# Performance work log

Hardware: AMD Instinct MI355X
Metric: run time of the kernel (lower is better)

The kernel has to match this reference:

```python
import jax, jax.numpy as jnp
import numpy as np

U = 256   # units
D = 256   # input_dim
B = 65536 # batch


def hard_tanh(x):
    return jnp.clip(x, -1.0, 1.0)


def binarize(x):
    # sign quantization (forward); straight-through in the bwd module
    return jnp.where(x >= 0, 1.0, -1.0).astype(x.dtype)


def setup_inputs() -> dict:
    key = jax.random.key(0)
    k1, k2, k3, k4, k5 = jax.random.split(key, 5)
    return {
        "inputs": jax.random.normal(k1, (B, D), dtype=jnp.float32),
        "h": jax.random.normal(k2, (B, U), dtype=jnp.float32),
        "c": jax.random.normal(k3, (B, U), dtype=jnp.float32),
        "kernel": jax.random.normal(k4, (D, 4 * U), dtype=jnp.float32) * 0.05,
        "recurrent_kernel": jax.random.normal(k5, (U, 4 * U), dtype=jnp.float32) * 0.05,
    }


def reference(inputs, h, c, kernel, recurrent_kernel):
    u = kernel.shape[1] // 4
    h_tm1 = hard_tanh(h)
    c_tm1 = hard_tanh(c)
    # binarized input projection, hard_tanh applied to each gate pre-activation
    x_all = hard_tanh(inputs @ binarize(kernel))            # [B, 4U]
    x_i, x_f, x_c, x_o = (x_all[:, :u], x_all[:, u:2*u],
                          x_all[:, 2*u:3*u], x_all[:, 3*u:])
    # binarized recurrent projection
    r_all = h_tm1 @ binarize(recurrent_kernel)              # [B, 4U]
    r_i, r_f, r_c, r_o = (r_all[:, :u], r_all[:, u:2*u],
                          r_all[:, 2*u:3*u], r_all[:, 3*u:])
    # NOTE: faithful to source: f pairs x_i with W_f, i pairs x_f with W_i
    f = hard_tanh(x_i + r_f)
    i = hard_tanh(x_f + r_i)
    c_new = f * c_tm1 + i * hard_tanh(x_c + r_c)
    o = hard_tanh(x_o + r_o)
    h_new = hard_tanh(o * hard_tanh(c_new))
    return (h_new, h_new, c_new)
```

## Files before the change

kernel.cpp:

```cpp
#include <hip/hip_runtime.h>


#define NB 65536

typedef _Float16 f16x8 __attribute__((ext_vector_type(8)));
typedef float f32x16 __attribute__((ext_vector_type(16)));

__device__ __forceinline__ float htanh(float x) { return fminf(1.f, fmaxf(-1.f, x)); }

__global__ void prep_w(const float* __restrict__ Kf, const float* __restrict__ RKf,
                       unsigned short* __restrict__ wfrag) {
  __shared__ unsigned short sgn[32][72];
  const int b = blockIdx.x;
  const int side = b >> 7, kt = (b >> 4) & 7, nt = b & 15;
  const float* M = side ? RKf : Kf;
  const int t = threadIdx.x;

  {
    const int k = t >> 3, n8 = (t & 7) << 3;
    const float* p = M + (kt * 32 + k) * 1024 + nt * 64 + n8;
    float4 v0 = *(const float4*)p;
    float4 v1 = *(const float4*)(p + 4);
    float xs[8] = {v0.x, v0.y, v0.z, v0.w, v1.x, v1.y, v1.z, v1.w};
#pragma unroll
    for (int i = 0; i < 8; ++i)
      sgn[k][n8 + i] = (xs[i] >= 0.f) ? 0x3C00u : 0xBC00u;
  }
  __syncthreads();

  const int fl = t >> 6, l = t & 63;
  const int j = fl >> 1, uh = fl & 1;
  const int nloc = uh * 32 + (l & 31);
  const int kloc = j * 16 + (l >> 5) * 8;
  unsigned short o[8];
#pragma unroll
  for (int e = 0; e < 8; ++e) o[e] = sgn[kloc + e][nloc];
  const int ng = nt * 64 + nloc;
  const int gate = ng >> 8, u32 = (ng >> 5) & 7;
  const int fragid = (((kt * 2 + j) * 2 + side) * 4 + gate) * 8 + u32;
  uint4 ov;
  ov.x = (unsigned)o[0] | ((unsigned)o[1] << 16);
  ov.y = (unsigned)o[2] | ((unsigned)o[3] << 16);
  ov.z = (unsigned)o[4] | ((unsigned)o[5] << 16);
  ov.w = (unsigned)o[6] | ((unsigned)o[7] << 16);
  *(uint4*)((char*)wfrag + fragid * 1024 + l * 16) = ov;
}

__global__ __launch_bounds__(256, 3)
void blstm_main(const float* __restrict__ xin, const float* __restrict__ hin,
                const float* __restrict__ cin, const unsigned short* __restrict__ wfrag,
                float* __restrict__ out) {
  __shared__ char smem[32768];

  const int bid = blockIdx.x;
  const int swz = (bid & 7) * 1024 + (bid >> 3);
  const int mb = swz >> 2, ub = swz & 3;
  const int m0 = mb << 5;
  const int u0 = ub << 6;

  const int tid = threadIdx.x;
  const int lane = tid & 63;
  const int w = tid >> 6;
  const int wu = w & 1, wg = w >> 1;
  const int l31 = lane & 31, lh = lane >> 5;

  const int sSide = tid >> 7;
  const int sRow = (tid & 127) >> 2;
  const int sQ = tid & 3;
  const float* aPtr = (sSide ? hin : xin) + (m0 + sRow) * 256 + (sQ << 3);
  char* const aWr = smem + sSide * 4096 + sRow * 128;
  const int swzHi = ((sQ ^ (sRow & 7)) << 4);
  const int swzLo = (((sQ + 4) ^ (sRow & 7)) << 4);

  const char* const wbase = (const char*)wfrag + lane * 16;

  f32x16 acc[4] = {};

  float4 a0 = *(const float4*)(aPtr);
  float4 a1 = *(const float4*)(aPtr + 4);

  for (int s = 0; s < 8; ++s) {
    {
      char* wr = aWr + (s & 1) * 8192;
      float xs[8] = {a0.x, a0.y, a0.z, a0.w, a1.x, a1.y, a1.z, a1.w};
      f16x8 hv, lv;
#pragma unroll
      for (int i = 0; i < 8; ++i) {
        float x = xs[i];
        if (sSide) x = htanh(x);
        _Float16 hf = (_Float16)x;
        hv[i] = hf;
        lv[i] = (_Float16)(x - (float)hf);
      }
      *(f16x8*)(wr + swzHi) = hv;
      *(f16x8*)(wr + swzLo) = lv;
    }

    f16x8 wfr[2][4];
#pragma unroll
    for (int j = 0; j < 2; ++j)
#pragma unroll
      for (int nf = 0; nf < 4; ++nf) {
        const int side = nf >> 1, gate = wg * 2 + (nf & 1);
        const int fragid = (((s * 2 + j) * 2 + side) * 4 + gate) * 8 + (ub * 2 + wu);
        wfr[j][nf] = *(const f16x8*)(wbase + fragid * 1024);
      }
    if (s < 7) {
      a0 = *(const float4*)(aPtr + (s + 1) * 32);
      a1 = *(const float4*)(aPtr + (s + 1) * 32 + 4);
    }

    __syncthreads();

    const char* rd = smem + (s & 1) * 8192;
#pragma unroll
    for (int j = 0; j < 2; ++j) {
#pragma unroll
      for (int hl = 0; hl < 2; ++hl) {
        f16x8 af[2];
#pragma unroll
        for (int side = 0; side < 2; ++side)
          af[side] = *(const f16x8*)(rd + side * 4096 + l31 * 128 +
                       ((((hl << 2) | (j << 1) | lh) ^ (l31 & 7)) << 4));
#pragma unroll
        for (int nf = 0; nf < 4; ++nf)
          acc[nf] = __builtin_amdgcn_mfma_f32_32x32x16_f16(af[nf >> 1], wfr[j][nf],
                                                           acc[nf], 0, 0, 0);
      }
    }
  }

  float* ex = (float*)(smem + 16384 + wu * 8192);

  if (wg == 1) {
    float4 c4[4], o4[4];
#pragma unroll
    for (int r = 0; r < 16; ++r) {
      float cand = htanh(htanh(acc[0][r]) + acc[2][r]);
      float og   = htanh(htanh(acc[1][r]) + acc[3][r]);
      ((float*)&c4[r >> 2])[r & 3] = cand;
      ((float*)&o4[r >> 2])[r & 3] = og;
    }
#pragma unroll
    for (int c = 0; c < 4; ++c) {
      *(float4*)((char*)ex + c * 1024 + lane * 16) = c4[c];
      *(float4*)((char*)ex + 4096 + c * 1024 + lane * 16) = o4[c];
    }
  }
  __syncthreads();
  if (wg == 0) {
    float4 c4[4], o4[4];
#pragma unroll
    for (int c = 0; c < 4; ++c) {
      c4[c] = *(const float4*)((const char*)ex + c * 1024 + lane * 16);
      o4[c] = *(const float4*)((const char*)ex + 4096 + c * 1024 + lane * 16);
    }
#pragma unroll
    for (int r = 0; r < 16; ++r) {
      const int row = (r & 3) + ((r >> 2) << 3) + (lh << 2);
      const int grow = m0 + row;
      const int gu = u0 + wu * 32 + l31;
      const float fg = htanh(htanh(acc[0][r]) + acc[3][r]);
      const float ig = htanh(htanh(acc[1][r]) + acc[2][r]);
      const float cand = ((const float*)&c4[r >> 2])[r & 3];
      const float og   = ((const float*)&o4[r >> 2])[r & 3];
      const float ct = htanh(cin[grow * 256 + gu]);
      const float cn = fg * ct + ig * cand;
      const float hn = htanh(og * htanh(cn));
      const int o1 = grow * 256 + gu;
      out[o1] = hn;
      out[NB * 256 + o1] = hn;
      out[2 * NB * 256 + o1] = cn;
    }
  }
}

extern "C" void kernel_launch(void* const* d_in, const int* in_sizes, int n_in,
                              void* d_out, int out_size, void* d_ws, size_t ws_size,
                              hipStream_t stream) {
  const float* xin = (const float*)d_in[0];
  const float* hin = (const float*)d_in[1];
  const float* cin = (const float*)d_in[2];
  const float* kf  = (const float*)d_in[3];
  const float* rkf = (const float*)d_in[4];
  float* out = (float*)d_out;

  unsigned short* wfrag = (unsigned short*)d_ws;

  prep_w<<<256, 256, 0, stream>>>(kf, rkf, wfrag);
  blstm_main<<<8192, 256, 0, stream>>>(xin, hin, cin, wfrag, out);
}
```

Measured before the change: 204.3 us.

## Split activation conversion into prep kernel and persistent register-resident GEMM

Adds a prep_a kernel that converts inputs and hard_tanh(h) into hi/lo fp16 MFMA fragment images in workspace. The main kernel becomes a persistent-style GEMM with 1024 blocks of 512 threads. Each wave keeps its weight fragments in registers across 8 row chunks and streams A fragments straight from global memory with double buffering, exchanging gate results through LDS. The weight fragment order is changed to suit this, and hard_tanh now uses fmed3. The cost is an extra round trip of the activation image (fp16 hi+lo, the same byte count as the fp32 source) through global memory, in exchange for removing LDS staging and the per-block reconversion.

```diff
diff --git a/kernel.cpp b/kernel.cpp
--- a/kernel.cpp
+++ b/kernel.cpp
@@ -4,9 +4,12 @@
 #define NB 65536
 
 typedef _Float16 f16x8 __attribute__((ext_vector_type(8)));
+typedef __fp16 fp16x2 __attribute__((ext_vector_type(2)));
 typedef float f32x16 __attribute__((ext_vector_type(16)));
 
-__device__ __forceinline__ float htanh(float x) { return fminf(1.f, fmaxf(-1.f, x)); }
+__device__ __forceinline__ float htanh(float x) {
+  return __builtin_amdgcn_fmed3f(x, -1.0f, 1.0f);
+}
 
 __global__ void prep_w(const float* __restrict__ Kf, const float* __restrict__ RKf,
                        unsigned short* __restrict__ wfrag) {
@@ -15,7 +18,6 @@
   const int side = b >> 7, kt = (b >> 4) & 7, nt = b & 15;
   const float* M = side ? RKf : Kf;
   const int t = threadIdx.x;
-
   {
     const int k = t >> 3, n8 = (t & 7) << 3;
     const float* p = M + (kt * 32 + k) * 1024 + nt * 64 + n8;
@@ -27,17 +29,17 @@
       sgn[k][n8 + i] = (xs[i] >= 0.f) ? 0x3C00u : 0xBC00u;
   }
   __syncthreads();
-
   const int fl = t >> 6, l = t & 63;
-  const int j = fl >> 1, uh = fl & 1;
-  const int nloc = uh * 32 + (l & 31);
+  const int j = fl >> 1, uhh = fl & 1;
+  const int nloc = uhh * 32 + (l & 31);
   const int kloc = j * 16 + (l >> 5) * 8;
   unsigned short o[8];
 #pragma unroll
   for (int e = 0; e < 8; ++e) o[e] = sgn[kloc + e][nloc];
   const int ng = nt * 64 + nloc;
   const int gate = ng >> 8, u32 = (ng >> 5) & 7;
-  const int fragid = (((kt * 2 + j) * 2 + side) * 4 + gate) * 8 + u32;
+  const int k16 = kt * 2 + j;
+  const int fragid = ((k16 * 2 + side) * 8 + u32) * 4 + gate;
   uint4 ov;
   ov.x = (unsigned)o[0] | ((unsigned)o[1] << 16);
   ov.y = (unsigned)o[2] | ((unsigned)o[3] << 16);
@@ -46,133 +48,190 @@
   *(uint4*)((char*)wfrag + fragid * 1024 + l * 16) = ov;
 }
 
-__global__ __launch_bounds__(256, 3)
-void blstm_main(const float* __restrict__ xin, const float* __restrict__ hin,
-                const float* __restrict__ cin, const unsigned short* __restrict__ wfrag,
-                float* __restrict__ out) {
-  __shared__ char smem[32768];
+__global__ __launch_bounds__(256)
+void prep_a(const float* __restrict__ xin, const float* __restrict__ hin,
+            char* __restrict__ aimg) {
+  __shared__ float tile[32][68];
+  const int b = blockIdx.x;
+  const int side = b & 1, kq = (b >> 1) & 3, strip = b >> 3;
+  const float* src = side ? hin : xin;
+  const int t = threadIdx.x;
+  {
+    const int row = t >> 3, kc = (t & 7) << 3;
+    const float* p = src + (strip * 32 + row) * 256 + kq * 64 + kc;
+    float4 v0 = *(const float4*)p;
+    float4 v1 = *(const float4*)(p + 4);
+    *(float4*)&tile[row][kc] = v0;
+    *(float4*)&tile[row][kc + 4] = v1;
+  }
+  __syncthreads();
+  const int w = t >> 6, l = t & 63;
+  const int l31 = l & 31, lh = l >> 5;
+  const int k16 = kq * 4 + w;
+  const int c0 = w * 16 + lh * 8;
+  float4 u0 = *(const float4*)&tile[l31][c0];
+  float4 u1 = *(const float4*)&tile[l31][c0 + 4];
+  float v0 = u0.x, v1 = u0.y, v2 = u0.z, v3 = u0.w;
+  float v4 = u1.x, v5 = u1.y, v6 = u1.z, v7 = u1.w;
+  if (side) {
+    v0 = htanh(v0); v1 = htanh(v1); v2 = htanh(v2); v3 = htanh(v3);
+    v4 = htanh(v4); v5 = htanh(v5); v6 = htanh(v6); v7 = htanh(v7);
+  }
+  fp16x2 h01 = __builtin_amdgcn_cvt_pkrtz(v0, v1);
+  fp16x2 h23 = __builtin_amdgcn_cvt_pkrtz(v2, v3);
+  fp16x2 h45 = __builtin_amdgcn_cvt_pkrtz(v4, v5);
+  fp16x2 h67 = __builtin_amdgcn_cvt_pkrtz(v6, v7);
+  fp16x2 l01 = __builtin_amdgcn_cvt_pkrtz(v0 - (float)h01[0], v1 - (float)h01[1]);
+  fp16x2 l23 = __builtin_amdgcn_cvt_pkrtz(v2 - (float)h23[0], v3 - (float)h23[1]);
+  fp16x2 l45 = __builtin_amdgcn_cvt_pkrtz(v4 - (float)h45[0], v5 - (float)h45[1]);
+  fp16x2 l67 = __builtin_amdgcn_cvt_pkrtz(v6 - (float)h67[0], v7 - (float)h67[1]);
+  uint4 H, L;
+  H.x = __builtin_bit_cast(unsigned, h01); H.y = __builtin_bit_cast(unsigned, h23);
+  H.z = __builtin_bit_cast(unsigned, h45); H.w = __builtin_bit_cast(unsigned, h67);
+  L.x = __builtin_bit_cast(unsigned, l01); L.y = __builtin_bit_cast(unsigned, l23);
+  L.z = __builtin_bit_cast(unsigned, l45); L.w = __builtin_bit_cast(unsigned, l67);
+  char* dst = aimg + (size_t)(((strip * 16 + k16) * 2 + side) * 2) * 1024 + l * 16;
+  *(uint4*)dst = H;
+  *(uint4*)(dst + 1024) = L;
+}
+
+__global__ __launch_bounds__(512, 4)
+void blstm_gemm(const char* __restrict__ aimg, const unsigned short* __restrict__ wfrag,
+                const float* __restrict__ cin, float* __restrict__ out) {
+  __shared__ char ex[65536];
 
   const int bid = blockIdx.x;
-  const int swz = (bid & 7) * 1024 + (bid >> 3);
-  const int mb = swz >> 2, ub = swz & 3;
-  const int m0 = mb << 5;
-  const int u0 = ub << 6;
-
-  const int tid = threadIdx.x;
-  const int lane = tid & 63;
-  const int w = tid >> 6;
-  const int wu = w & 1, wg = w >> 1;
+  const int xcd = bid & 7, j = bid >> 3;
+  const int U = j & 7, g8 = j >> 3;
+  const int tid = threadIdx.x, lane = tid & 63, w = tid >> 6;
+  const int s = w & 1, gate = w >> 1;
   const int l31 = lane & 31, lh = lane >> 5;
 
-  const int sSide = tid >> 7;
-  const int sRow = (tid & 127) >> 2;
-  const int sQ = tid & 3;
-  const float* aPtr = (sSide ? hin : xin) + (m0 + sRow) * 256 + (sQ << 3);
-  char* const aWr = smem + sSide * 4096 + sRow * 128;
-  const int swzHi = ((sQ ^ (sRow & 7)) << 4);
-  const int swzLo = (((sQ + 4) ^ (sRow & 7)) << 4);
-
-  const char* const wbase = (const char*)wfrag + lane * 16;
-
-  f32x16 acc[4] = {};
-
-  float4 a0 = *(const float4*)(aPtr);
-  float4 a1 = *(const float4*)(aPtr + 4);
-
-  for (int s = 0; s < 8; ++s) {
-    {
-      char* wr = aWr + (s & 1) * 8192;
-      float xs[8] = {a0.x, a0.y, a0.z, a0.w, a1.x, a1.y, a1.z, a1.w};
-      f16x8 hv, lv;
-#pragma unroll
-      for (int i = 0; i < 8; ++i) {
-        float x = xs[i];
-        if (sSide) x = htanh(x);
-        _Float16 hf = (_Float16)x;
-        hv[i] = hf;
-        lv[i] = (_Float16)(x - (float)hf);
+  const char* wb = (const char*)wfrag + s * 32768 + U * 4096 + gate * 1024 + lane * 16;
+  const char* ab0 = aimg + s * 2048 + lane * 16;
+
+  const int chunk0 = xcd * 128 + g8 * 8;
+
+  f16x8 wreg[8];
+  f32x16 acc[2];
+  f16x8 a0h, a0l, a1h, a1l, b0h, b0l, b1h, b1l;
+
+#define AADDR(C, ST, K, T) (ab0 + (size_t)((C) * 2 + (ST)) * 65536 + (K) * 4096 + (T) * 1024)
+
+#pragma unroll
+  for (int k = 0; k < 8; ++k) wreg[k] = *(const f16x8*)(wb + k * 65536);
+  a0h = *(const f16x8*)AADDR(chunk0, 0, 0, 0);
+  a0l = *(const f16x8*)AADDR(chunk0, 0, 0, 1);
+  a1h = *(const f16x8*)AADDR(chunk0, 1, 0, 0);
+  a1l = *(const f16x8*)AADDR(chunk0, 1, 0, 1);
+
+#define MFMA_STEP(CH0, CL0, CH1, CL1, WF) do {                                \
+    acc[0] = __builtin_amdgcn_mfma_f32_32x32x16_f16(CH0, WF, acc[0], 0, 0, 0); \
+    acc[0] = __builtin_amdgcn_mfma_f32_32x32x16_f16(CL0, WF, acc[0], 0, 0, 0); \
+    acc[1] = __builtin_amdgcn_mfma_f32_32x32x16_f16(CH1, WF, acc[1], 0, 0, 0); \
+    acc[1] = __builtin_amdgcn_mfma_f32_32x32x16_f16(CL1, WF, acc[1], 0, 0, 0); \
+  } while (0)
+
+#define KS(K, C0H, C0L, C1H, C1L, N0H, N0L, N1H, N1L) do {                    \
+    if ((K) < 15) {                                                           \
+      N0H = *(const f16x8*)AADDR(chunk, 0, (K) + 1, 0);                       \
+      N0L = *(const f16x8*)AADDR(chunk, 0, (K) + 1, 1);                       \
+      N1H = *(const f16x8*)AADDR(chunk, 1, (K) + 1, 0);                       \
+      N1L = *(const f16x8*)AADDR(chunk, 1, (K) + 1, 1);                       \
+    } else if (t < 7) {                                                       \
+      N0H = *(const f16x8*)AADDR(chunk + 1, 0, 0, 0);                         \
+      N0L = *(const f16x8*)AADDR(chunk + 1, 0, 0, 1);                         \
+      N1H = *(const f16x8*)AADDR(chunk + 1, 1, 0, 0);                         \
+      N1L = *(const f16x8*)AADDR(chunk + 1, 1, 0, 1);                         \
+    }                                                                         \
+    MFMA_STEP(C0H, C0L, C1H, C1L, wreg[(K) & 7]);                             \
+    if ((K) == 7) {                                                           \
+      _Pragma("unroll")                                                       \
+      for (int kk = 0; kk < 8; ++kk)                                          \
+        wreg[kk] = *(const f16x8*)(wb + (8 + kk) * 65536);                    \
+    }                                                                         \
+    if ((K) == 15 && t < 7) {                                                 \
+      _Pragma("unroll")                                                       \
+      for (int kk = 0; kk < 8; ++kk)                                          \
+        wreg[kk] = *(const f16x8*)(wb + kk * 65536);                          \
+    }                                                                         \
+  } while (0)
+
+#pragma unroll 1
+  for (int t = 0; t < 8; ++t) {
+    const int chunk = chunk0 + t;
+    const int m0 = chunk * 64;
+    const f32x16 zacc = {};
+    acc[0] = zacc;
+    acc[1] = zacc;
+
+    KS(0,  a0h, a0l, a1h, a1l,  b0h, b0l, b1h, b1l);
+    KS(1,  b0h, b0l, b1h, b1l,  a0h, a0l, a1h, a1l);
+    KS(2,  a0h, a0l, a1h, a1l,  b0h, b0l, b1h, b1l);
+    KS(3,  b0h, b0l, b1h, b1l,  a0h, a0l, a1h, a1l);
+    KS(4,  a0h, a0l, a1h, a1l,  b0h, b0l, b1h, b1l);
+    KS(5,  b0h, b0l, b1h, b1l,  a0h, a0l, a1h, a1l);
+    KS(6,  a0h, a0l, a1h, a1l,  b0h, b0l, b1h, b1l);
+    KS(7,  b0h, b0l, b1h, b1l,  a0h, a0l, a1h, a1l);
+    KS(8,  a0h, a0l, a1h, a1l,  b0h, b0l, b1h, b1l);
+    KS(9,  b0h, b0l, b1h, b1l,  a0h, a0l, a1h, a1l);
+    KS(10, a0h, a0l, a1h, a1l,  b0h, b0l, b1h, b1l);
+    KS(11, b0h, b0l, b1h, b1l,  a0h, a0l, a1h, a1l);
+    KS(12, a0h, a0l, a1h, a1l,  b0h, b0l, b1h, b1l);
+    KS(13, b0h, b0l, b1h, b1l,  a0h, a0l, a1h, a1l);
+    KS(14, a0h, a0l, a1h, a1l,  b0h, b0l, b1h, b1l);
+    KS(15, b0h, b0l, b1h, b1l,  a0h, a0l, a1h, a1l);
+
+    const int Rb = w * 8 + lh * 4;
+    float ct0 = cin[(m0 + Rb + 0) * 256 + U * 32 + l31];
+    float ct1 = cin[(m0 + Rb + 1) * 256 + U * 32 + l31];
+    float ct2 = cin[(m0 + Rb + 2) * 256 + U * 32 + l31];
+    float ct3 = cin[(m0 + Rb + 3) * 256 + U * 32 + l31];
+
+    asm volatile("s_waitcnt lgkmcnt(0)\n\ts_barrier" ::: "memory");
+#pragma unroll
+    for (int st = 0; st < 2; ++st)
+#pragma unroll
+      for (int q = 0; q < 4; ++q) {
+        float4 v;
+        v.x = acc[st][q * 4 + 0]; v.y = acc[st][q * 4 + 1];
+        v.z = acc[st][q * 4 + 2]; v.w = acc[st][q * 4 + 3];
+        *(float4*)(ex + w * 8192 + st * 4096 + q * 1024 + lane * 16) = v;
       }
-      *(f16x8*)(wr + swzHi) = hv;
-      *(f16x8*)(wr + swzLo) = lv;
+    asm volatile("s_waitcnt lgkmcnt(0)\n\ts_barrier" ::: "memory");
+
+    float cts[4] = {ct0, ct1, ct2, ct3};
+#pragma unroll
+    for (int i = 0; i < 4; ++i) {
+      const int R = Rb + i;
+      const int st = R >> 5, r32 = R & 31;
+      const int q = r32 >> 3, el = r32 & 3;
+      const int sl = l31 + ((r32 >> 2) & 1) * 32;
+      const int off = st * 4096 + q * 1024 + sl * 16 + el * 4;
+      const float xi = htanh(*(const float*)(ex + 0 * 8192 + off));
+      const float ri =        *(const float*)(ex + 1 * 8192 + off);
+      const float xf = htanh(*(const float*)(ex + 2 * 8192 + off));
+      const float rf =        *(const float*)(ex + 3 * 8192 + off);
+      const float xc = htanh(*(const float*)(ex + 4 * 8192 + off));
+      const float rc =        *(const float*)(ex + 5 * 8192 + off);
+      const float xo = htanh(*(const float*)(ex + 6 * 8192 + off));
+      const float ro =        *(const float*)(ex + 7 * 8192 + off);
+      const float fg   = htanh(xi + rf);
+      const float ig   = htanh(xf + ri);
+      const float cand = htanh(xc + rc);
+      const float og   = htanh(xo + ro);
+      const float c0 = htanh(cts[i]);
+      const float cn = fg * c0 + ig * cand;
+      const float hn = htanh(og * htanh(cn));
+      const int o1 = (m0 + R) * 256 + U * 32 + l31;
+      out[o1] = hn;
+      out[16777216 + o1] = hn;
+      out[33554432 + o1] = cn;
     }
-
-    f16x8 wfr[2][4];
-#pragma unroll
-    for (int j = 0; j < 2; ++j)
-#pragma unroll
-      for (int nf = 0; nf < 4; ++nf) {
-        const int side = nf >> 1, gate = wg * 2 + (nf & 1);
-        const int fragid = (((s * 2 + j) * 2 + side) * 4 + gate) * 8 + (ub * 2 + wu);
-        wfr[j][nf] = *(const f16x8*)(wbase + fragid * 1024);
-      }
-    if (s < 7) {
-      a0 = *(const float4*)(aPtr + (s + 1) * 32);
-      a1 = *(const float4*)(aPtr + (s + 1) * 32 + 4);
-    }
-
-    __syncthreads();
-
-    const char* rd = smem + (s & 1) * 8192;
-#pragma unroll
-    for (int j = 0; j < 2; ++j) {
-#pragma unroll
-      for (int hl = 0; hl < 2; ++hl) {
-        f16x8 af[2];
-#pragma unroll
-        for (int side = 0; side < 2; ++side)
-          af[side] = *(const f16x8*)(rd + side * 4096 + l31 * 128 +
-                       ((((hl << 2) | (j << 1) | lh) ^ (l31 & 7)) << 4));
-#pragma unroll
-        for (int nf = 0; nf < 4; ++nf)
-          acc[nf] = __builtin_amdgcn_mfma_f32_32x32x16_f16(af[nf >> 1], wfr[j][nf],
-                                                           acc[nf], 0, 0, 0);
-      }
-    }
-  }
-
-  float* ex = (float*)(smem + 16384 + wu * 8192);
-
-  if (wg == 1) {
-    float4 c4[4], o4[4];
-#pragma unroll
-    for (int r = 0; r < 16; ++r) {
-      float cand = htanh(htanh(acc[0][r]) + acc[2][r]);
-      float og   = htanh(htanh(acc[1][r]) + acc[3][r]);
-      ((float*)&c4[r >> 2])[r & 3] = cand;
-      ((float*)&o4[r >> 2])[r & 3] = og;
-    }
-#pragma unroll
-    for (int c = 0; c < 4; ++c) {
-      *(float4*)((char*)ex + c * 1024 + lane * 16) = c4[c];
-      *(float4*)((char*)ex + 4096 + c * 1024 + lane * 16) = o4[c];
-    }
-  }
-  __syncthreads();
-  if (wg == 0) {
-    float4 c4[4], o4[4];
-#pragma unroll
-    for (int c = 0; c < 4; ++c) {
-      c4[c] = *(const float4*)((const char*)ex + c * 1024 + lane * 16);
-      o4[c] = *(const float4*)((const char*)ex + 4096 + c * 1024 + lane * 16);
-    }
-#pragma unroll
-    for (int r = 0; r < 16; ++r) {
-      const int row = (r & 3) + ((r >> 2) << 3) + (lh << 2);
-      const int grow = m0 + row;
-      const int gu = u0 + wu * 32 + l31;
-      const float fg = htanh(htanh(acc[0][r]) + acc[3][r]);
-      const float ig = htanh(htanh(acc[1][r]) + acc[2][r]);
-      const float cand = ((const float*)&c4[r >> 2])[r & 3];
-      const float og   = ((const float*)&o4[r >> 2])[r & 3];
-      const float ct = htanh(cin[grow * 256 + gu]);
-      const float cn = fg * ct + ig * cand;
-      const float hn = htanh(og * htanh(cn));
-      const int o1 = grow * 256 + gu;
-      out[o1] = hn;
-      out[NB * 256 + o1] = hn;
-      out[2 * NB * 256 + o1] = cn;
-    }
-  }
+  }
+#undef KS
+#undef MFMA_STEP
+#undef AADDR
 }
 
 extern "C" void kernel_launch(void* const* d_in, const int* in_sizes, int n_in,
@@ -186,7 +245,9 @@
   float* out = (float*)d_out;
 
   unsigned short* wfrag = (unsigned short*)d_ws;
+  char* aimg = (char*)d_ws + (1 << 20);
 
   prep_w<<<256, 256, 0, stream>>>(kf, rkf, wfrag);
-  blstm_main<<<8192, 256, 0, stream>>>(xin, hin, cin, wfrag, out);
-}
+  prep_a<<<16384, 256, 0, stream>>>(xin, hin, aimg);
+  blstm_gemm<<<1024, 512, 0, stream>>>(aimg, wfrag, cin, out);
+}
```

Measured after the change: 541.5 us. 165% more time.

## Rewrite fused BLSTM GEMM with 64-row tiles, persistent loop, register double-buffered weights

Applied to the files above, without the earlier changes.

Replaces the main kernel with a version that processes 64-row M tiles (two per block over a persistent loop of 2048 blocks), double-buffers the weight fragments in registers and the activation tiles in shared memory, and uses packed fp16 conversion, fmed3 clamping, setprio around MFMA bursts and raw barriers. The gate-exchange epilogue is reorganized so the other wave group computes the output and prefetches c earlier. The goal is better weight reuse per load, fewer launched blocks, and overlap of global loads with MFMA work. In exchange it uses more LDS and registers, which lowers occupancy to 2 blocks per SM, and it uses round-toward-zero packing for the hi/lo fp16 split.

```diff
diff --git a/kernel.cpp b/kernel.cpp
--- a/kernel.cpp
+++ b/kernel.cpp
@@ -4,9 +4,17 @@
 #define NB 65536
 
 typedef _Float16 f16x8 __attribute__((ext_vector_type(8)));
+typedef __fp16 fp16x2 __attribute__((ext_vector_type(2)));
 typedef float f32x16 __attribute__((ext_vector_type(16)));
 
-__device__ __forceinline__ float htanh(float x) { return fminf(1.f, fmaxf(-1.f, x)); }
+__device__ __forceinline__ float htanh(float x) {
+  return __builtin_amdgcn_fmed3f(x, -1.0f, 1.0f);
+}
+
+__device__ __forceinline__ unsigned pk2(float a, float b) {
+  fp16x2 p = __builtin_amdgcn_cvt_pkrtz(a, b);
+  return __builtin_bit_cast(unsigned, p);
+}
 
 __global__ void prep_w(const float* __restrict__ Kf, const float* __restrict__ RKf,
                        unsigned short* __restrict__ wfrag) {
@@ -15,7 +23,6 @@
   const int side = b >> 7, kt = (b >> 4) & 7, nt = b & 15;
   const float* M = side ? RKf : Kf;
   const int t = threadIdx.x;
-
   {
     const int k = t >> 3, n8 = (t & 7) << 3;
     const float* p = M + (kt * 32 + k) * 1024 + nt * 64 + n8;
@@ -27,17 +34,17 @@
       sgn[k][n8 + i] = (xs[i] >= 0.f) ? 0x3C00u : 0xBC00u;
   }
   __syncthreads();
-
   const int fl = t >> 6, l = t & 63;
-  const int j = fl >> 1, uh = fl & 1;
-  const int nloc = uh * 32 + (l & 31);
+  const int j = fl >> 1, uhh = fl & 1;
+  const int nloc = uhh * 32 + (l & 31);
   const int kloc = j * 16 + (l >> 5) * 8;
   unsigned short o[8];
 #pragma unroll
   for (int e = 0; e < 8; ++e) o[e] = sgn[kloc + e][nloc];
   const int ng = nt * 64 + nloc;
   const int gate = ng >> 8, u32 = (ng >> 5) & 7;
-  const int fragid = (((kt * 2 + j) * 2 + side) * 4 + gate) * 8 + u32;
+  const int k16 = kt * 2 + j;
+  const int fragid = ((k16 * 2 + side) * 8 + u32) * 4 + gate;
   uint4 ov;
   ov.x = (unsigned)o[0] | ((unsigned)o[1] << 16);
   ov.y = (unsigned)o[2] | ((unsigned)o[3] << 16);
@@ -46,133 +53,196 @@
   *(uint4*)((char*)wfrag + fragid * 1024 + l * 16) = ov;
 }
 
-__global__ __launch_bounds__(256, 3)
-void blstm_main(const float* __restrict__ xin, const float* __restrict__ hin,
+__global__ __launch_bounds__(256, 2)
+void blstm_gemm(const float* __restrict__ xin, const float* __restrict__ hin,
                 const float* __restrict__ cin, const unsigned short* __restrict__ wfrag,
                 float* __restrict__ out) {
-  __shared__ char smem[32768];
+  __shared__ char smem[65536];
 
   const int bid = blockIdx.x;
-  const int swz = (bid & 7) * 1024 + (bid >> 3);
-  const int mb = swz >> 2, ub = swz & 3;
-  const int m0 = mb << 5;
-  const int u0 = ub << 6;
-
-  const int tid = threadIdx.x;
-  const int lane = tid & 63;
-  const int w = tid >> 6;
-  const int wu = w & 1, wg = w >> 1;
+  const int swz = (bid & 7) * 256 + (bid >> 3);
+  const int U = swz & 3;
+  const int mg = swz >> 2;
+
+  const int tid = threadIdx.x, lane = tid & 63, w = tid >> 6;
+  const int gp = w >> 1, uhf = w & 1;
   const int l31 = lane & 31, lh = lane >> 5;
 
   const int sSide = tid >> 7;
-  const int sRow = (tid & 127) >> 2;
-  const int sQ = tid & 3;
-  const float* aPtr = (sSide ? hin : xin) + (m0 + sRow) * 256 + (sQ << 3);
-  char* const aWr = smem + sSide * 4096 + sRow * 128;
-  const int swzHi = ((sQ ^ (sRow & 7)) << 4);
-  const int swzLo = (((sQ + 4) ^ (sRow & 7)) << 4);
-
-  const char* const wbase = (const char*)wfrag + lane * 16;
-
-  f32x16 acc[4] = {};
-
-  float4 a0 = *(const float4*)(aPtr);
-  float4 a1 = *(const float4*)(aPtr + 4);
-
-  for (int s = 0; s < 8; ++s) {
-    {
-      char* wr = aWr + (s & 1) * 8192;
-      float xs[8] = {a0.x, a0.y, a0.z, a0.w, a1.x, a1.y, a1.z, a1.w};
-      f16x8 hv, lv;
-#pragma unroll
-      for (int i = 0; i < 8; ++i) {
-        float x = xs[i];
-        if (sSide) x = htanh(x);
-        _Float16 hf = (_Float16)x;
-        hv[i] = hf;
-        lv[i] = (_Float16)(x - (float)hf);
-      }
-      *(f16x8*)(wr + swzHi) = hv;
-      *(f16x8*)(wr + swzLo) = lv;
+  const int sRow = (tid & 127) >> 1;
+  const int sKh = tid & 1;
+  const float* const aP0 = (sSide ? hin : xin) + (size_t)sRow * 256 + sKh * 16;
+  char* const swr = smem +
+      ((((sKh * 2 + sSide) * 2 + (sRow >> 5)) * 2) * 1024) + (sRow & 31) * 16;
+
+  const char* const wq = (const char*)wfrag + lane * 16;
+  int wbOff[4];
+#pragma unroll
+  for (int nf = 0; nf < 4; ++nf) {
+    const int side = nf >> 1, gate = gp * 2 + (nf & 1);
+    wbOff[nf] = (side * 32 + (U * 2 + uhf) * 4 + gate) * 1024;
+  }
+
+  f32x16 acc[2][4];
+  f16x8 wA[8], wB[8];
+  float4 av0, av1, av2, av3;
+
+#pragma unroll
+  for (int j = 0; j < 2; ++j)
+#pragma unroll
+    for (int nf = 0; nf < 4; ++nf)
+      wA[j * 4 + nf] = *(const f16x8*)(wq + (0 + j) * 65536 + wbOff[nf]);
+
+#define CVT_STORE(B) do {                                                    \
+    float e_[16] = {av0.x, av0.y, av0.z, av0.w, av1.x, av1.y, av1.z, av1.w,  \
+                    av2.x, av2.y, av2.z, av2.w, av3.x, av3.y, av3.z, av3.w}; \
+    if (sSide) {                                                             \
+      _Pragma("unroll") for (int i_ = 0; i_ < 16; ++i_) e_[i_] = htanh(e_[i_]); \
+    }                                                                        \
+    unsigned hw_[8], lw_[8];                                                 \
+    _Pragma("unroll")                                                        \
+    for (int i_ = 0; i_ < 8; ++i_) {                                         \
+      fp16x2 h_ = __builtin_amdgcn_cvt_pkrtz(e_[2 * i_], e_[2 * i_ + 1]);    \
+      hw_[i_] = __builtin_bit_cast(unsigned, h_);                            \
+      lw_[i_] = pk2(e_[2 * i_] - (float)h_[0], e_[2 * i_ + 1] - (float)h_[1]); \
+    }                                                                        \
+    char* wp_ = swr + (B) * 16384;                                           \
+    *(uint4*)(wp_)        = make_uint4(hw_[0], hw_[1], hw_[2], hw_[3]);      \
+    *(uint4*)(wp_ + 512)  = make_uint4(hw_[4], hw_[5], hw_[6], hw_[7]);      \
+    *(uint4*)(wp_ + 1024) = make_uint4(lw_[0], lw_[1], lw_[2], lw_[3]);      \
+    *(uint4*)(wp_ + 1536) = make_uint4(lw_[4], lw_[5], lw_[6], lw_[7]);      \
+  } while (0)
+
+#define K16(J, WARR, RB) do {                                                \
+    _Pragma("unroll")                                                        \
+    for (int sd_ = 0; sd_ < 2; ++sd_) {                                      \
+      _Pragma("unroll")                                                      \
+      for (int st_ = 0; st_ < 2; ++st_) {                                    \
+        f16x8 ah_ = *(const f16x8*)((RB) + (J) * 8192 + sd_ * 4096 + st_ * 2048); \
+        f16x8 al_ = *(const f16x8*)((RB) + (J) * 8192 + sd_ * 4096 + st_ * 2048 + 1024); \
+        acc[st_][sd_ * 2 + 0] = __builtin_amdgcn_mfma_f32_32x32x16_f16(      \
+            ah_, WARR[(J) * 4 + sd_ * 2 + 0], acc[st_][sd_ * 2 + 0], 0, 0, 0); \
+        acc[st_][sd_ * 2 + 1] = __builtin_amdgcn_mfma_f32_32x32x16_f16(      \
+            ah_, WARR[(J) * 4 + sd_ * 2 + 1], acc[st_][sd_ * 2 + 1], 0, 0, 0); \
+        acc[st_][sd_ * 2 + 0] = __builtin_amdgcn_mfma_f32_32x32x16_f16(      \
+            al_, WARR[(J) * 4 + sd_ * 2 + 0], acc[st_][sd_ * 2 + 0], 0, 0, 0); \
+        acc[st_][sd_ * 2 + 1] = __builtin_amdgcn_mfma_f32_32x32x16_f16(      \
+            al_, WARR[(J) * 4 + sd_ * 2 + 1], acc[st_][sd_ * 2 + 1], 0, 0, 0); \
+      }                                                                      \
+    }                                                                        \
+  } while (0)
+
+#define STEP(S, WCUR, WNXT, LAST) do {                                       \
+    asm volatile("s_waitcnt lgkmcnt(0)\n\ts_barrier" ::: "memory");          \
+    if (!(LAST)) {                                                           \
+      av0 = *(const float4*)(aPc + ((S) + 1) * 32);                          \
+      av1 = *(const float4*)(aPc + ((S) + 1) * 32 + 4);                      \
+      av2 = *(const float4*)(aPc + ((S) + 1) * 32 + 8);                      \
+      av3 = *(const float4*)(aPc + ((S) + 1) * 32 + 12);                     \
+    }                                                                        \
+    _Pragma("unroll")                                                        \
+    for (int j_ = 0; j_ < 2; ++j_)                                           \
+      _Pragma("unroll")                                                      \
+      for (int nf_ = 0; nf_ < 4; ++nf_)                                      \
+        WNXT[j_ * 4 + nf_] = *(const f16x8*)(                                \
+            wq + (((((S) + 1) & 7) * 2) + j_) * 65536 + wbOff[nf_]);         \
+    {                                                                        \
+      const char* rb_ = smem + ((S) & 1) * 16384 + lane * 16;                \
+      __builtin_amdgcn_s_setprio(1);                                         \
+      K16(0, WCUR, rb_);                                                     \
+      K16(1, WCUR, rb_);                                                     \
+      __builtin_amdgcn_s_setprio(0);                                         \
+    }                                                                        \
+    if (!(LAST)) CVT_STORE(((S) + 1) & 1);                                   \
+  } while (0)
+
+  float* ex = (float*)(smem + 32768);
+
+#pragma unroll 1
+  for (int c = 0; c < 2; ++c) {
+    const int m0 = (mg + c * 512) * 64;
+    const float* aPc = aP0 + (size_t)m0 * 256;
+
+    const f32x16 z = {};
+#pragma unroll
+    for (int st = 0; st < 2; ++st)
+#pragma unroll
+      for (int nf = 0; nf < 4; ++nf) acc[st][nf] = z;
+
+    av0 = *(const float4*)(aPc);
+    av1 = *(const float4*)(aPc + 4);
+    av2 = *(const float4*)(aPc + 8);
+    av3 = *(const float4*)(aPc + 12);
+    CVT_STORE(0);
+
+    STEP(0, wA, wB, false);
+    STEP(1, wB, wA, false);
+    STEP(2, wA, wB, false);
+    STEP(3, wB, wA, false);
+    STEP(4, wA, wB, false);
+    STEP(5, wB, wA, false);
+    STEP(6, wA, wB, false);
+    STEP(7, wB, wA, true);
+
+    const int uc = U * 64 + uhf * 32 + l31;
+    float cins[32];
+    if (gp == 1) {
+#pragma unroll
+      for (int st = 0; st < 2; ++st)
+#pragma unroll
+        for (int q = 0; q < 4; ++q)
+#pragma unroll
+          for (int i = 0; i < 4; ++i) {
+            const int row = st * 32 + 8 * q + 4 * lh + i;
+            cins[(st * 4 + q) * 4 + i] = cin[(size_t)(m0 + row) * 256 + uc];
+          }
     }
-
-    f16x8 wfr[2][4];
-#pragma unroll
-    for (int j = 0; j < 2; ++j)
-#pragma unroll
-      for (int nf = 0; nf < 4; ++nf) {
-        const int side = nf >> 1, gate = wg * 2 + (nf & 1);
-        const int fragid = (((s * 2 + j) * 2 + side) * 4 + gate) * 8 + (ub * 2 + wu);
-        wfr[j][nf] = *(const f16x8*)(wbase + fragid * 1024);
-      }
-    if (s < 7) {
-      a0 = *(const float4*)(aPtr + (s + 1) * 32);
-      a1 = *(const float4*)(aPtr + (s + 1) * 32 + 4);
+    if (gp == 0) {
+#pragma unroll
+      for (int st = 0; st < 2; ++st)
+#pragma unroll
+        for (int q = 0; q < 4; ++q) {
+          float4 fv, iv;
+#pragma unroll
+          for (int i = 0; i < 4; ++i) {
+            const int r = q * 4 + i;
+            ((float*)&fv)[i] = htanh(htanh(acc[st][0][r]) + acc[st][3][r]);
+            ((float*)&iv)[i] = htanh(htanh(acc[st][1][r]) + acc[st][2][r]);
+          }
+          *(float4*)((char*)ex + (((uhf * 2 + 0) * 2 + st) * 4096) + q * 1024 + lane * 16) = fv;
+          *(float4*)((char*)ex + (((uhf * 2 + 1) * 2 + st) * 4096) + q * 1024 + lane * 16) = iv;
+        }
     }
-
-    __syncthreads();
-
-    const char* rd = smem + (s & 1) * 8192;
-#pragma unroll
-    for (int j = 0; j < 2; ++j) {
-#pragma unroll
-      for (int hl = 0; hl < 2; ++hl) {
-        f16x8 af[2];
-#pragma unroll
-        for (int side = 0; side < 2; ++side)
-          af[side] = *(const f16x8*)(rd + side * 4096 + l31 * 128 +
-                       ((((hl << 2) | (j << 1) | lh) ^ (l31 & 7)) << 4));
-#pragma unroll
-        for (int nf = 0; nf < 4; ++nf)
-          acc[nf] = __builtin_amdgcn_mfma_f32_32x32x16_f16(af[nf >> 1], wfr[j][nf],
-                                                           acc[nf], 0, 0, 0);
-      }
+    asm volatile("s_waitcnt lgkmcnt(0)\n\ts_barrier" ::: "memory");
+    if (gp == 1) {
+#pragma unroll
+      for (int st = 0; st < 2; ++st)
+#pragma unroll
+        for (int q = 0; q < 4; ++q) {
+          float4 fv = *(const float4*)((char*)ex + (((uhf * 2 + 0) * 2 + st) * 4096) + q * 1024 + lane * 16);
+          float4 iv = *(const float4*)((char*)ex + (((uhf * 2 + 1) * 2 + st) * 4096) + q * 1024 + lane * 16);
+#pragma unroll
+          for (int i = 0; i < 4; ++i) {
+            const int r = q * 4 + i;
+            const float cand = htanh(htanh(acc[st][0][r]) + acc[st][2][r]);
+            const float og   = htanh(htanh(acc[st][1][r]) + acc[st][3][r]);
+            const float fg = ((const float*)&fv)[i];
+            const float ig = ((const float*)&iv)[i];
+            const float ct = htanh(cins[(st * 4 + q) * 4 + i]);
+            const float cn = fg * ct + ig * cand;
+            const float hn = htanh(og * htanh(cn));
+            const int row = st * 32 + 8 * q + 4 * lh + i;
+            const size_t o1 = (size_t)(m0 + row) * 256 + uc;
+            out[o1] = hn;
+            out[(size_t)NB * 256 + o1] = hn;
+            out[2 * (size_t)NB * 256 + o1] = cn;
+          }
+        }
     }
   }
-
-  float* ex = (float*)(smem + 16384 + wu * 8192);
-
-  if (wg == 1) {
-    float4 c4[4], o4[4];
-#pragma unroll
-    for (int r = 0; r < 16; ++r) {
-      float cand = htanh(htanh(acc[0][r]) + acc[2][r]);
-      float og   = htanh(htanh(acc[1][r]) + acc[3][r]);
-      ((float*)&c4[r >> 2])[r & 3] = cand;
-      ((float*)&o4[r >> 2])[r & 3] = og;
-    }
-#pragma unroll
-    for (int c = 0; c < 4; ++c) {
-      *(float4*)((char*)ex + c * 1024 + lane * 16) = c4[c];
-      *(float4*)((char*)ex + 4096 + c * 1024 + lane * 16) = o4[c];
-    }
-  }
-  __syncthreads();
-  if (wg == 0) {
-    float4 c4[4], o4[4];
-#pragma unroll
-    for (int c = 0; c < 4; ++c) {
-      c4[c] = *(const float4*)((const char*)ex + c * 1024 + lane * 16);
-      o4[c] = *(const float4*)((const char*)ex + 4096 + c * 1024 + lane * 16);
-    }
-#pragma unroll
-    for (int r = 0; r < 16; ++r) {
-      const int row = (r & 3) + ((r >> 2) << 3) + (lh << 2);
-      const int grow = m0 + row;
-      const int gu = u0 + wu * 32 + l31;
-      const float fg = htanh(htanh(acc[0][r]) + acc[3][r]);
-      const float ig = htanh(htanh(acc[1][r]) + acc[2][r]);
-      const float cand = ((const float*)&c4[r >> 2])[r & 3];
-      const float og   = ((const float*)&o4[r >> 2])[r & 3];
-      const float ct = htanh(cin[grow * 256 + gu]);
-      const float cn = fg * ct + ig * cand;
-      const float hn = htanh(og * htanh(cn));
-      const int o1 = grow * 256 + gu;
-      out[o1] = hn;
-      out[NB * 256 + o1] = hn;
-      out[2 * NB * 256 + o1] = cn;
-    }
-  }
+#undef STEP
+#undef K16
+#undef CVT_STORE
 }
 
 extern "C" void kernel_launch(void* const* d_in, const int* in_sizes, int n_in,
@@ -188,5 +258,5 @@
   unsigned short* wfrag = (unsigned short*)d_ws;
 
   prep_w<<<256, 256, 0, stream>>>(kf, rkf, wfrag);
-  blstm_main<<<8192, 256, 0, stream>>>(xin, hin, cin, wfrag, out);
-}
+  blstm_gemm<<<2048, 256, 0, stream>>>(xin, hin, cin, wfrag, out);
+}
```

New measurement: 522.4 us. 2.56x slower.

## Rewrite BLSTM kernel with 256x32 tiles, LDS-staged weights and software pipeline

Applied to the files above, without the earlier changes.

Replaces the 32-row by 64-unit tiling with 256-row by 32-unit tiles per 512-thread block, so each weight fragment is reused across eight times more rows. Weights are staged in double-buffered LDS, and the A/B loads are pipelined two steps ahead in a fully unrolled 16-step loop with MFMA priority hints. The epilogue now writes per-gate results through LDS so each thread emits coalesced float4 stores. The weight-prep kernel is also reorganised. The cost is 155KB of dynamic LDS and one block per CU, which leaves only in-block pipelining to hide latency.

```diff
diff --git a/kernel.cpp b/kernel.cpp
--- a/kernel.cpp
+++ b/kernel.cpp
@@ -4,174 +4,231 @@
 #define NB 65536
 
 typedef _Float16 f16x8 __attribute__((ext_vector_type(8)));
+typedef __fp16 fp16x2 __attribute__((ext_vector_type(2)));
 typedef float f32x16 __attribute__((ext_vector_type(16)));
 
-__device__ __forceinline__ float htanh(float x) { return fminf(1.f, fmaxf(-1.f, x)); }
-
-__global__ void prep_w(const float* __restrict__ Kf, const float* __restrict__ RKf,
-                       unsigned short* __restrict__ wfrag) {
-  __shared__ unsigned short sgn[32][72];
+__device__ __forceinline__ float htanh(float x) {
+  return __builtin_amdgcn_fmed3f(x, -1.0f, 1.0f);
+}
+
+__global__ __launch_bounds__(512)
+void prep_w(const float* __restrict__ Kf, const float* __restrict__ RKf,
+            char* __restrict__ wimg) {
   const int b = blockIdx.x;
-  const int side = b >> 7, kt = (b >> 4) & 7, nt = b & 15;
+  const int s = b & 15;
+  const int side = s >> 3, ks = s & 7;
   const float* M = side ? RKf : Kf;
   const int t = threadIdx.x;
-
-  {
-    const int k = t >> 3, n8 = (t & 7) << 3;
-    const float* p = M + (kt * 32 + k) * 1024 + nt * 64 + n8;
-    float4 v0 = *(const float4*)p;
-    float4 v1 = *(const float4*)(p + 4);
-    float xs[8] = {v0.x, v0.y, v0.z, v0.w, v1.x, v1.y, v1.z, v1.w};
-#pragma unroll
-    for (int i = 0; i < 8; ++i)
-      sgn[k][n8 + i] = (xs[i] >= 0.f) ? 0x3C00u : 0xBC00u;
-  }
-  __syncthreads();
-
-  const int fl = t >> 6, l = t & 63;
-  const int j = fl >> 1, uh = fl & 1;
-  const int nloc = uh * 32 + (l & 31);
-  const int kloc = j * 16 + (l >> 5) * 8;
+  const int kh = t >> 8, gate = (t >> 6) & 3, l = t & 63;
+  const int nb = b >> 4;
+  const int col = gate * 256 + nb * 32 + (l & 31);
+  const int k0 = ks * 32 + kh * 16 + (l >> 5) * 8;
   unsigned short o[8];
 #pragma unroll
-  for (int e = 0; e < 8; ++e) o[e] = sgn[kloc + e][nloc];
-  const int ng = nt * 64 + nloc;
-  const int gate = ng >> 8, u32 = (ng >> 5) & 7;
-  const int fragid = (((kt * 2 + j) * 2 + side) * 4 + gate) * 8 + u32;
+  for (int e = 0; e < 8; ++e)
+    o[e] = (M[(k0 + e) * 1024 + col] >= 0.f) ? 0x3C00u : 0xBC00u;
   uint4 ov;
   ov.x = (unsigned)o[0] | ((unsigned)o[1] << 16);
   ov.y = (unsigned)o[2] | ((unsigned)o[3] << 16);
   ov.z = (unsigned)o[4] | ((unsigned)o[5] << 16);
   ov.w = (unsigned)o[6] | ((unsigned)o[7] << 16);
-  *(uint4*)((char*)wfrag + fragid * 1024 + l * 16) = ov;
-}
-
-__global__ __launch_bounds__(256, 3)
+  *(uint4*)(wimg + (size_t)b * 8192 + kh * 4096 + gate * 1024 + l * 16) = ov;
+}
+
+__global__ __launch_bounds__(512, 1)
 void blstm_main(const float* __restrict__ xin, const float* __restrict__ hin,
-                const float* __restrict__ cin, const unsigned short* __restrict__ wfrag,
+                const float* __restrict__ cin, const char* __restrict__ wimg,
                 float* __restrict__ out) {
-  __shared__ char smem[32768];
+  extern __shared__ char smem0[];
 
   const int bid = blockIdx.x;
-  const int swz = (bid & 7) * 1024 + (bid >> 3);
-  const int mb = swz >> 2, ub = swz & 3;
-  const int m0 = mb << 5;
-  const int u0 = ub << 6;
-
-  const int tid = threadIdx.x;
-  const int lane = tid & 63;
-  const int w = tid >> 6;
-  const int wu = w & 1, wg = w >> 1;
+  const int xcd = bid & 7, ii = bid >> 3;
+  const int mb = xcd * 32 + (ii >> 3), nb = ii & 7;
+  const int m0 = mb << 8;
+
+  const int tid = threadIdx.x, lane = tid & 63, w = tid >> 6;
+  const int mw = w >> 1, nw = w & 1;
   const int l31 = lane & 31, lh = lane >> 5;
 
-  const int sSide = tid >> 7;
-  const int sRow = (tid & 127) >> 2;
-  const int sQ = tid & 3;
-  const float* aPtr = (sSide ? hin : xin) + (m0 + sRow) * 256 + (sQ << 3);
-  char* const aWr = smem + sSide * 4096 + sRow * 128;
-  const int swzHi = ((sQ ^ (sRow & 7)) << 4);
-  const int swzLo = (((sQ + 4) ^ (sRow & 7)) << 4);
-
-  const char* const wbase = (const char*)wfrag + lane * 16;
-
-  f32x16 acc[4] = {};
-
-  float4 a0 = *(const float4*)(aPtr);
-  float4 a1 = *(const float4*)(aPtr + 4);
-
-  for (int s = 0; s < 8; ++s) {
+  const int sRow = tid >> 1, sKh = tid & 1;
+  const int sMf = sRow >> 5, sL31 = sRow & 31;
+  const int sSlot = (sL31 & 24) | ((sL31 ^ sMf) & 7);
+  const float* const xrow = xin + (size_t)(m0 + sRow) * 256 + sKh * 16;
+  const float* const hrow = hin + (size_t)(m0 + sRow) * 256 + sKh * 16;
+  char* const aWrBase = smem0 + sMf * 1024 + sSlot * 16;
+  const char* const wstep = wimg + (size_t)(nb * 16) * 8192 + tid * 16;
+
+  const int lh512 = lh * 512;
+  const int slotA0 = (l31 & 24) | ((l31 ^ (mw * 2 + 0)) & 7);
+  const int slotA1 = (l31 & 24) | ((l31 ^ (mw * 2 + 1)) & 7);
+  const int aOff0 = (mw * 2 + 0) * 1024 + slotA0 * 16;
+  const int aOff1 = (mw * 2 + 1) * 1024 + slotA1 * 16;
+  const int bOff0 = (nw * 2 + 0) * 1024 + lane * 16;
+  const int bOff1 = (nw * 2 + 1) * 1024 + lane * 16;
+
+  f32x16 acc[2][2][2] = {};
+  uint4 bvA, bvB;
+  float4 paA0, paA1, paA2, paA3, paB0, paB1, paB2, paB3;
+
+#define BLOAD(BV, SP) BV = *(const uint4*)(wstep + (size_t)(SP) * 8192)
+
+#define ALOADX(P0, P1, P2, P3, SP) do {                                       \
+    const float* p_ = (((SP) >= 8) ? hrow : xrow) + ((SP) & 7) * 32;          \
+    P0 = *(const float4*)(p_);      P1 = *(const float4*)(p_ + 4);            \
+    P2 = *(const float4*)(p_ + 8);  P3 = *(const float4*)(p_ + 12);           \
+  } while (0)
+
+#define BSTORE(BV, SN) \
+    *(uint4*)(smem0 + 65536 + ((SN) & 1) * 8192 + tid * 16) = BV
+
+#define ACVT(P0, P1, P2, P3, SN) do {                                         \
+    float e_[16] = {(P0).x, (P0).y, (P0).z, (P0).w,                           \
+                    (P1).x, (P1).y, (P1).z, (P1).w,                           \
+                    (P2).x, (P2).y, (P2).z, (P2).w,                           \
+                    (P3).x, (P3).y, (P3).z, (P3).w};                          \
+    if ((SN) >= 8) {                                                          \
+      _Pragma("unroll") for (int i_ = 0; i_ < 16; ++i_) e_[i_] = htanh(e_[i_]); \
+    }                                                                         \
+    unsigned hw_[8], lw_[8];                                                  \
+    _Pragma("unroll")                                                         \
+    for (int i_ = 0; i_ < 8; ++i_) {                                          \
+      fp16x2 h_ = __builtin_amdgcn_cvt_pkrtz(e_[2*i_], e_[2*i_+1]);           \
+      hw_[i_] = __builtin_bit_cast(unsigned, h_);                             \
+      fp16x2 l_ = __builtin_amdgcn_cvt_pkrtz(e_[2*i_]   - (float)h_[0],       \
+                                             e_[2*i_+1] - (float)h_[1]);      \
+      lw_[i_] = __builtin_bit_cast(unsigned, l_);                             \
+    }                                                                         \
+    char* b_ = aWrBase + ((SN) & 1) * 32768;                                  \
+    *(uint4*)(b_ + sKh * 8192)             = make_uint4(hw_[0], hw_[1], hw_[2], hw_[3]); \
+    *(uint4*)(b_ + sKh * 8192 + 512)       = make_uint4(hw_[4], hw_[5], hw_[6], hw_[7]); \
+    *(uint4*)(b_ + (2 + sKh) * 8192)       = make_uint4(lw_[0], lw_[1], lw_[2], lw_[3]); \
+    *(uint4*)(b_ + (2 + sKh) * 8192 + 512) = make_uint4(lw_[4], lw_[5], lw_[6], lw_[7]); \
+  } while (0)
+
+#define MM(AF, BF, AC) AC = __builtin_amdgcn_mfma_f32_32x32x16_f16(AF, BF, AC, 0, 0, 0)
+
+#define COMP(S) do {                                                          \
+    const char* a_ = smem0 + ((S) & 1) * 32768 + lh512;                       \
+    const char* b_ = smem0 + 65536 + ((S) & 1) * 8192;                        \
+    f16x8 B00 = *(const f16x8*)(b_ + bOff0);                                  \
+    f16x8 B01 = *(const f16x8*)(b_ + bOff1);                                  \
+    f16x8 B10 = *(const f16x8*)(b_ + 4096 + bOff0);                           \
+    f16x8 B11 = *(const f16x8*)(b_ + 4096 + bOff1);                           \
+    f16x8 A00 = *(const f16x8*)(a_ + 0 * 8192 + aOff0);                       \
+    f16x8 A01 = *(const f16x8*)(a_ + 0 * 8192 + aOff1);                       \
+    f16x8 A20 = *(const f16x8*)(a_ + 2 * 8192 + aOff0);                       \
+    f16x8 A21 = *(const f16x8*)(a_ + 2 * 8192 + aOff1);                       \
+    f16x8 A10 = *(const f16x8*)(a_ + 1 * 8192 + aOff0);                       \
+    f16x8 A11 = *(const f16x8*)(a_ + 1 * 8192 + aOff1);                       \
+    f16x8 A30 = *(const f16x8*)(a_ + 3 * 8192 + aOff0);                       \
+    f16x8 A31 = *(const f16x8*)(a_ + 3 * 8192 + aOff1);                       \
+    f32x16* ac = &acc[(S) >> 3][0][0];                                        \
+    __builtin_amdgcn_s_setprio(1);                                            \
+    MM(A00, B00, ac[0]); MM(A00, B01, ac[1]);                                 \
+    MM(A01, B00, ac[2]); MM(A01, B01, ac[3]);                                 \
+    MM(A20, B00, ac[0]); MM(A20, B01, ac[1]);                                 \
+    MM(A21, B00, ac[2]); MM(A21, B01, ac[3]);                                 \
+    MM(A10, B10, ac[0]); MM(A10, B11, ac[1]);                                 \
+    MM(A11, B10, ac[2]); MM(A11, B11, ac[3]);                                 \
+    MM(A30, B10, ac[0]); MM(A30, B11, ac[1]);                                 \
+    MM(A31, B10, ac[2]); MM(A31, B11, ac[3]);                                 \
+    __builtin_amdgcn_s_setprio(0);                                            \
+  } while (0)
+
+#define STEP(S, BVC, C0, C1, C2, C3, BVN, N0, N1, N2, N3) do {                \
+    if ((S) < 14) { BLOAD(BVN, (S) + 2); ALOADX(N0, N1, N2, N3, (S) + 2); }   \
+    if ((S) < 15) { BSTORE(BVC, (S) + 1); ACVT(C0, C1, C2, C3, (S) + 1); }    \
+    COMP(S);                                                                  \
+    if ((S) < 15)                                                             \
+      asm volatile("s_waitcnt lgkmcnt(0)\n\ts_barrier" ::: "memory");         \
+  } while (0)
+
+  BLOAD(bvA, 0); ALOADX(paA0, paA1, paA2, paA3, 0);
+  BLOAD(bvB, 1); ALOADX(paB0, paB1, paB2, paB3, 1);
+  BSTORE(bvA, 0); ACVT(paA0, paA1, paA2, paA3, 0);
+  asm volatile("s_waitcnt lgkmcnt(0)\n\ts_barrier" ::: "memory");
+
+  STEP(0,  bvB, paB0, paB1, paB2, paB3, bvA, paA0, paA1, paA2, paA3);
+  STEP(1,  bvA, paA0, paA1, paA2, paA3, bvB, paB0, paB1, paB2, paB3);
+  STEP(2,  bvB, paB0, paB1, paB2, paB3, bvA, paA0, paA1, paA2, paA3);
+  STEP(3,  bvA, paA0, paA1, paA2, paA3, bvB, paB0, paB1, paB2, paB3);
+  STEP(4,  bvB, paB0, paB1, paB2, paB3, bvA, paA0, paA1, paA2, paA3);
+  STEP(5,  bvA, paA0, paA1, paA2, paA3, bvB, paB0, paB1, paB2, paB3);
+  STEP(6,  bvB, paB0, paB1, paB2, paB3, bvA, paA0, paA1, paA2, paA3);
+  STEP(7,  bvA, paA0, paA1, paA2, paA3, bvB, paB0, paB1, paB2, paB3);
+  STEP(8,  bvB, paB0, paB1, paB2, paB3, bvA, paA0, paA1, paA2, paA3);
+  STEP(9,  bvA, paA0, paA1, paA2, paA3, bvB, paB0, paB1, paB2, paB3);
+  STEP(10, bvB, paB0, paB1, paB2, paB3, bvA, paA0, paA1, paA2, paA3);
+  STEP(11, bvA, paA0, paA1, paA2, paA3, bvB, paB0, paB1, paB2, paB3);
+  STEP(12, bvB, paB0, paB1, paB2, paB3, bvA, paA0, paA1, paA2, paA3);
+  STEP(13, bvA, paA0, paA1, paA2, paA3, bvB, paB0, paB1, paB2, paB3);
+  STEP(14, bvB, paB0, paB1, paB2, paB3, bvA, paA0, paA1, paA2, paA3);
+  STEP(15, bvA, paA0, paA1, paA2, paA3, bvB, paB0, paB1, paB2, paB3);
+
+#undef STEP
+#undef COMP
+#undef MM
+#undef ACVT
+#undef BSTORE
+#undef ALOADX
+#undef BLOAD
+
+  float* const exf = (float*)(smem0 + 81920);
+  const int rowl = tid >> 3, u4g = (tid & 7) * 4;
+
+#pragma unroll 1
+  for (int p = 0; p < 4; ++p) {
+    if (mw == p) {
+#pragma unroll
+      for (int side = 0; side < 2; ++side)
+#pragma unroll
+        for (int mfl = 0; mfl < 2; ++mfl)
+#pragma unroll
+          for (int nfl = 0; nfl < 2; ++nfl) {
+            const int sgW = side * 4 + nw * 2 + nfl;
+            float* bp = exf + sgW * 2304 + (mfl * 32 + lh * 4) * 36 + l31;
+#pragma unroll
+            for (int q = 0; q < 4; ++q)
+#pragma unroll
+              for (int rl = 0; rl < 4; ++rl)
+                bp[(q * 8 + rl) * 36] = acc[side][mfl][nfl][q * 4 + rl];
+          }
+    }
+    const size_t obase = (size_t)(m0 + p * 64 + rowl) * 256 + nb * 32 + u4g;
+    float4 cv = *(const float4*)(cin + obase);
+    __syncthreads();
     {
-      char* wr = aWr + (s & 1) * 8192;
-      float xs[8] = {a0.x, a0.y, a0.z, a0.w, a1.x, a1.y, a1.z, a1.w};
-      f16x8 hv, lv;
-#pragma unroll
-      for (int i = 0; i < 8; ++i) {
-        float x = xs[i];
-        if (sSide) x = htanh(x);
-        _Float16 hf = (_Float16)x;
-        hv[i] = hf;
-        lv[i] = (_Float16)(x - (float)hf);
+      const float* rp = exf + rowl * 36 + u4g;
+      float4 v0 = *(const float4*)(rp + 0 * 2304);
+      float4 v1 = *(const float4*)(rp + 1 * 2304);
+      float4 v2 = *(const float4*)(rp + 2 * 2304);
+      float4 v3 = *(const float4*)(rp + 3 * 2304);
+      float4 v4 = *(const float4*)(rp + 4 * 2304);
+      float4 v5 = *(const float4*)(rp + 5 * 2304);
+      float4 v6 = *(const float4*)(rp + 6 * 2304);
+      float4 v7 = *(const float4*)(rp + 7 * 2304);
+      float4 ho, co;
+#pragma unroll
+      for (int j = 0; j < 4; ++j) {
+        const float xi = htanh(((const float*)&v0)[j]);
+        const float xf = htanh(((const float*)&v1)[j]);
+        const float xc = htanh(((const float*)&v2)[j]);
+        const float xo = htanh(((const float*)&v3)[j]);
+        const float fg   = htanh(xi + ((const float*)&v5)[j]);
+        const float ig   = htanh(xf + ((const float*)&v4)[j]);
+        const float cand = htanh(xc + ((const float*)&v6)[j]);
+        const float og   = htanh(xo + ((const float*)&v7)[j]);
+        const float ct = htanh(((const float*)&cv)[j]);
+        const float cn = fg * ct + ig * cand;
+        const float hn = htanh(og * htanh(cn));
+        ((float*)&ho)[j] = hn;
+        ((float*)&co)[j] = cn;
       }
-      *(f16x8*)(wr + swzHi) = hv;
-      *(f16x8*)(wr + swzLo) = lv;
+      *(float4*)(out + obase) = ho;
+      *(float4*)(out + (size_t)NB * 256 + obase) = ho;
+      *(float4*)(out + 2 * (size_t)NB * 256 + obase) = co;
     }
-
-    f16x8 wfr[2][4];
-#pragma unroll
-    for (int j = 0; j < 2; ++j)
-#pragma unroll
-      for (int nf = 0; nf < 4; ++nf) {
-        const int side = nf >> 1, gate = wg * 2 + (nf & 1);
-        const int fragid = (((s * 2 + j) * 2 + side) * 4 + gate) * 8 + (ub * 2 + wu);
-        wfr[j][nf] = *(const f16x8*)(wbase + fragid * 1024);
-      }
-    if (s < 7) {
-      a0 = *(const float4*)(aPtr + (s + 1) * 32);
-      a1 = *(const float4*)(aPtr + (s + 1) * 32 + 4);
-    }
-
     __syncthreads();
-
-    const char* rd = smem + (s & 1) * 8192;
-#pragma unroll
-    for (int j = 0; j < 2; ++j) {
-#pragma unroll
-      for (int hl = 0; hl < 2; ++hl) {
-        f16x8 af[2];
-#pragma unroll
-        for (int side = 0; side < 2; ++side)
-          af[side] = *(const f16x8*)(rd + side * 4096 + l31 * 128 +
-                       ((((hl << 2) | (j << 1) | lh) ^ (l31 & 7)) << 4));
-#pragma unroll
-        for (int nf = 0; nf < 4; ++nf)
-          acc[nf] = __builtin_amdgcn_mfma_f32_32x32x16_f16(af[nf >> 1], wfr[j][nf],
-                                                           acc[nf], 0, 0, 0);
-      }
-    }
-  }
-
-  float* ex = (float*)(smem + 16384 + wu * 8192);
-
-  if (wg == 1) {
-    float4 c4[4], o4[4];
-#pragma unroll
-    for (int r = 0; r < 16; ++r) {
-      float cand = htanh(htanh(acc[0][r]) + acc[2][r]);
-      float og   = htanh(htanh(acc[1][r]) + acc[3][r]);
-      ((float*)&c4[r >> 2])[r & 3] = cand;
-      ((float*)&o4[r >> 2])[r & 3] = og;
-    }
-#pragma unroll
-    for (int c = 0; c < 4; ++c) {
-      *(float4*)((char*)ex + c * 1024 + lane * 16) = c4[c];
-      *(float4*)((char*)ex + 4096 + c * 1024 + lane * 16) = o4[c];
-    }
-  }
-  __syncthreads();
-  if (wg == 0) {
-    float4 c4[4], o4[4];
-#pragma unroll
-    for (int c = 0; c < 4; ++c) {
-      c4[c] = *(const float4*)((const char*)ex + c * 1024 + lane * 16);
-      o4[c] = *(const float4*)((const char*)ex + 4096 + c * 1024 + lane * 16);
-    }
-#pragma unroll
-    for (int r = 0; r < 16; ++r) {
-      const int row = (r & 3) + ((r >> 2) << 3) + (lh << 2);
-      const int grow = m0 + row;
-      const int gu = u0 + wu * 32 + l31;
-      const float fg = htanh(htanh(acc[0][r]) + acc[3][r]);
-      const float ig = htanh(htanh(acc[1][r]) + acc[2][r]);
-      const float cand = ((const float*)&c4[r >> 2])[r & 3];
-      const float og   = ((const float*)&o4[r >> 2])[r & 3];
-      const float ct = htanh(cin[grow * 256 + gu]);
-      const float cn = fg * ct + ig * cand;
-      const float hn = htanh(og * htanh(cn));
-      const int o1 = grow * 256 + gu;
-      out[o1] = hn;
-      out[NB * 256 + o1] = hn;
-      out[2 * NB * 256 + o1] = cn;
-    }
   }
 }
 
@@ -185,8 +242,11 @@
   const float* rkf = (const float*)d_in[4];
   float* out = (float*)d_out;
 
-  unsigned short* wfrag = (unsigned short*)d_ws;
-
-  prep_w<<<256, 256, 0, stream>>>(kf, rkf, wfrag);
-  blstm_main<<<8192, 256, 0, stream>>>(xin, hin, cin, wfrag, out);
-}
+  char* wimg = (char*)d_ws;
+
+  (void)hipFuncSetAttribute((const void*)blstm_main,
+                            hipFuncAttributeMaxDynamicSharedMemorySize, 155648);
+
+  prep_w<<<128, 512, 0, stream>>>(kf, rkf, wimg);
+  blstm_main<<<2048, 512, 155648, stream>>>(xin, hin, cin, wimg, out);
+}
```

Result: no change. 207.4 us (+1.5%).
